# Kernel tuning notes

Measured on AMD Instinct MI355X. Metric: run time of the kernel, lower is better.

## Reference

```python
import jax, jax.numpy as jnp
import numpy as np

B, C, H, W = 4, 96, 256, 256
HEADS = 4
WH = WW = 8            # window size
QKV_D = C // HEADS     # qkv_dim defaults to in_channels // num_heads
N = WH * WW            # tokens per window
EPS = 1e-6


def _rel_index():
    # Swin-style relative position index, [N, N], constant
    coords = np.stack(np.meshgrid(np.arange(WH), np.arange(WW), indexing='ij'), 0).reshape(2, -1)
    rel = coords[:, :, None] - coords[:, None, :]
    rel[0] += WH - 1
    rel[1] += WW - 1
    return rel[0] * (2 * WW - 1) + rel[1]

REL = jnp.asarray(_rel_index())  # int32 [N, N]


def setup_inputs() -> dict:
    key = jax.random.key(0)
    ks = jax.random.split(key, 8)
    s = lambda k, shape: jax.random.normal(k, shape, jnp.float32) * 0.02
    return dict(
        x=jax.random.normal(ks[0], (B, C, H, W), jnp.float32),
        norm_w=jnp.ones((C,), jnp.float32),                      # RMSNorm inside MHA (channel-last tokens)
        qkv_w=s(ks[1], (3 * HEADS * QKV_D, C)),
        qkv_b=jnp.zeros((3 * HEADS * QKV_D,), jnp.float32),
        proj_w=s(ks[2], (C, HEADS * QKV_D)),
        proj_b=jnp.zeros((C,), jnp.float32),
        bias_table=s(ks[3], ((2 * WH - 1) * (2 * WW - 1),)),     # WindowScoreBias table (shared across heads)
        mlp_norm_w=jnp.ones((1, C, 1, 1), jnp.float32),          # RMSNorm1((1,C,1,1), dim=1)
        w1_w=s(ks[4], (2 * C, C, 1, 1)),                         # mid = out_channels*mlp_ratio = 2C
        w1_b=jnp.zeros((2 * C,), jnp.float32),
        w2_w=s(ks[5], (C, C, 3, 3)),                             # mid//2 = C -> C, 3x3
        w2_b=jnp.zeros((C,), jnp.float32),
    )


def rms_norm(x, w, axis):
    v = jnp.mean(x * x, axis=axis, keepdims=True)
    return x * jax.lax.rsqrt(v + EPS) * w


def conv2d(x, w, b):
    y = jax.lax.conv_general_dilated(x, w, (1, 1), 'VALID',
                                     dimension_numbers=('NCHW', 'OIHW', 'NCHW'))
    return y + b[None, :, None, None]


def reference(x, norm_w, qkv_w, qkv_b, proj_w, proj_b, bias_table,
              mlp_norm_w, w1_w, w1_b, w2_w, w2_b):
    B_, C_, H_, W_ = x.shape
    nH, nW = H_ // WH, W_ // WW
    # ---- windowed MHA with norm fused in and relative bias ----
    # window partition: [B,C,H,W] -> [B*nWin, N, C]
    xw = x.reshape(B_, C_, nH, WH, nW, WW).transpose(0, 2, 4, 3, 5, 1).reshape(-1, N, C_)
    xn = rms_norm(xw, norm_w, -1)
    qkv = xn @ qkv_w.T + qkv_b                                  # [Bn, N, 3*h*d]
    qkv = qkv.reshape(-1, N, 3, HEADS, QKV_D).transpose(2, 0, 3, 1, 4)  # [3, Bn, h, N, d]
    q, k, v = qkv[0], qkv[1], qkv[2]
    bias = bias_table[REL]                                      # [N, N], broadcast over batch/heads
    scores = jnp.einsum('bhnd,bhmd->bhnm', q, k) / jnp.sqrt(jnp.float32(QKV_D)) + bias
    attn = jax.nn.softmax(scores, axis=-1)
    o = jnp.einsum('bhnm,bhmd->bhnd', attn, v)
    o = o.transpose(0, 2, 1, 3).reshape(-1, N, HEADS * QKV_D)
    o = o @ proj_w.T + proj_b
    # reverse window partition
    o = o.reshape(B_, nH, nW, WH, WW, C_).transpose(0, 5, 1, 3, 2, 4).reshape(B_, C_, H_, W_)
    x = x + o
    # ---- GLU conv MLP residual ----
    y = rms_norm(x, mlp_norm_w, 1)
    y = conv2d(y, w1_w, w1_b)                                   # 1x1, C -> 2C
    a, g = jnp.split(y, 2, axis=1)
    y = a * jax.nn.sigmoid(g)                                   # GLU along channels
    # ReplicationPad2dDetach: edge pad whose padded ring carries no gradient
    yp = jnp.pad(jax.lax.stop_gradient(y), ((0, 0), (0, 0), (1, 1), (1, 1)), mode='edge')
    yp = yp.at[:, :, 1:-1, 1:-1].set(y)
    y = conv2d(yp, w2_w, w2_b)                                  # 3x3 valid on padded -> same size
    y = jnp.where(y >= 0, y, 0.1 * y)                           # leaky_relu(0.1)
    return x + y
```

## Files before the change

kernel.cpp:

```cpp
#include <hip/hip_runtime.h>
#include <hip/hip_bf16.h>

#define CC 96

typedef short short8  __attribute__((ext_vector_type(8)));
typedef short short4v __attribute__((ext_vector_type(4)));
typedef float f32x4   __attribute__((ext_vector_type(4)));
typedef _Float16 half4 __attribute__((ext_vector_type(4)));

#if __has_builtin(__builtin_amdgcn_mfma_f32_16x16x16_f16)
  #define MFMA16(a,b,c) __builtin_amdgcn_mfma_f32_16x16x16_f16((a),(b),(c),0,0,0)
#else
  #define MFMA16(a,b,c) __builtin_amdgcn_mfma_f32_16x16x16f16((a),(b),(c),0,0,0)
#endif

static __device__ __forceinline__ ushort f2bf(float f) {
  __hip_bfloat16 h = __float2bfloat16(f);
  return *reinterpret_cast<ushort*>(&h);
}
static __device__ __forceinline__ float bf2f(ushort u) {
  union { unsigned int u; float f; } v; v.u = ((unsigned int)u) << 16; return v.f;
}

#define QSCALE 0.20412414523193154f

__global__ void prep_kernel(const float* __restrict__ qkv_w,
                            const float* __restrict__ qkv_b,
                            const float* __restrict__ proj_w,
                            const float* __restrict__ w2w,
                            const float* __restrict__ w1w,
                            __hip_bfloat16* __restrict__ qkvp,
                            float* __restrict__ qkvb2,
                            __hip_bfloat16* __restrict__ projp,
                            __hip_bfloat16* __restrict__ w2p,
                            __hip_bfloat16* __restrict__ w1p,
                            __hip_bfloat16* __restrict__ vwp)
{
  const int i = blockIdx.x*256 + threadIdx.x;
  if (i < 36864) {
    const int e = i & 7, lane = (i >> 3) & 63;
    const int rest = i >> 9;
    const int mt = rest % 6, r2 = rest / 6;
    const int ks = r2 % 3, h = r2 / 3;
    const int od = mt*16 + (lane & 15);
    const int sec = od >> 5, d = od & 31;
    const int c = ks*32 + (lane >> 4)*8 + e;
    float val = 0.f;
    if (d < 24) {
      val = qkv_w[(sec*96 + h*24 + d)*96 + c];
      if (sec == 0) val *= QSCALE;
    }
    qkvp[i] = __float2bfloat16(val);
  }
  const int jb = i - 36864;
  if (jb >= 0 && jb < 384) {
    const int h = jb / 96, od = jb - h*96;
    const int sec = od >> 5, d = od & 31;
    float val = 0.f;
    if (d < 24) {
      val = qkv_b[sec*96 + h*24 + d];
      if (sec == 0) val *= QSCALE;
    }
    qkvb2[jb] = val;
  }
  const int j = i - 37248;
  if (j >= 0 && j < 9216) {
    const int e = j & 7, lane = (j >> 3) & 63;
    const int rest = j >> 9;
    const int nt = rest % 6, ks = rest / 6;
    const int oc = nt*16 + (lane & 15);
    const int dd = ks*32 + (lane >> 4)*8 + e;
    projp[j] = __float2bfloat16(proj_w[oc*96 + dd]);
  }
  const int k = i - 46464;
  if (k >= 0 && k < 82944) {
    const int e = k & 7;
    const int lane = (k >> 3) & 63;
    const int rest = k >> 9;
    const int nf = rest % 6;
    const int r2 = rest / 6;
    const int kc = r2 % 3;
    const int tap = r2 / 3;
    const int cidx = kc*32 + (lane >> 4)*8 + e;
    const int oc = nf*16 + (lane & 15);
    const int ky = tap / 3, kx = tap - ky*3;
    w2p[k] = __float2bfloat16(w2w[((oc*96 + cidx)*3 + ky)*3 + kx]);
  }
  const int m = i - 129408;
  if (m >= 0 && m < 18432) {
    const int e = m & 7, lane = (m >> 3) & 63;
    const int rest = m >> 9;
    const int nt = rest % 12, ks = rest / 12;
    const int oc = nt*16 + (lane & 15);
    const int c  = ks*32 + (lane >> 4)*8 + e;
    w1p[m] = __float2bfloat16(w1w[oc*96 + c]);
  }
  const int v = i - 147840;
  if (v >= 0 && v < 12288) {
    const int e = v & 7, lane = (v >> 3) & 63;
    const int rest = v >> 9;
    const int nt2 = rest % 2, r2 = rest / 2;
    const int ks = r2 % 3, h = r2 / 3;
    const int d = nt2*16 + (lane & 15);
    const int c = ks*32 + (lane >> 4)*8 + e;
    const float val = (d < 24) ? qkv_w[(192 + h*24 + d)*96 + c] : 0.f;
    vwp[v] = __float2bfloat16(val);
  }
}

__global__ __launch_bounds__(512, 2) void attn_kernel(
    const float* __restrict__ x,
    const float* __restrict__ norm_w,
    const __hip_bfloat16* __restrict__ qkvp,
    const float* __restrict__ qkvb2,
    const __hip_bfloat16* __restrict__ vwp,
    const __hip_bfloat16* __restrict__ projp,
    const float* __restrict__ proj_b,
    const float* __restrict__ bias_table,
    float* __restrict__ out)
{
  extern __shared__ char smem[];
  ushort* xn   = (ushort*)smem;
  ushort* xr   = (ushort*)(smem + 26624);
  float*  btab = (float*)(smem + 51200);

  const int wp = blockIdx.x;
  const int b   = wp >> 9;
  const int wy  = (wp >> 4) & 31;
  const int wxp = wp & 15;
  const int t  = threadIdx.x;
  const int y0 = wy*8, x0 = wxp*16;
  const int l  = t & 63;
  const int W  = __builtin_amdgcn_readfirstlane(t >> 6);
  const int w2 = W >> 2, h = W & 3;
  const int lr = l & 15, g = l >> 4;

  for (int i = t; i < 225; i += 512) btab[i] = bias_table[i];

  {
    const int p = t >> 2, q = t & 3;
    const int ty = p >> 4, tx = p & 15;
    const float* xp = x + (size_t)(b*CC + q*24)*65536 + (size_t)(y0+ty)*256 + x0 + tx;
    float xv[24]; float ss = 0.f;
    #pragma unroll
    for (int i = 0; i < 24; i++) { xv[i] = xp[(size_t)i*65536]; ss += xv[i]*xv[i]; }
    ss += __shfl_xor(ss, 1);
    ss += __shfl_xor(ss, 2);
    const float s = rsqrtf(ss * (1.f/96.f) + 1e-6f);
    const int row = (tx >> 3)*64 + ty*8 + (tx & 7);
    #pragma unroll
    for (int k2 = 0; k2 < 3; k2++) {
      short8 pk, pr;
      #pragma unroll
      for (int q2 = 0; q2 < 8; q2++) {
        pr[q2] = (short)f2bf(xv[k2*8+q2]);
        pk[q2] = (short)f2bf(xv[k2*8+q2] * s * norm_w[q*24 + k2*8 + q2]);
      }
      *(short8*)(xn + row*104 + q*24 + k2*8) = pk;
      *(short8*)(xr + row*96  + q*24 + k2*8) = pr;
    }
  }
  __syncthreads();

  half4 qf[2][4], kf[2][4];
  #pragma unroll
  for (int pass = 0; pass < 2; pass++) {
    f32x4 acc[2][4];
    #pragma unroll
    for (int m2 = 0; m2 < 2; m2++)
      #pragma unroll
      for (int nt = 0; nt < 4; nt++) acc[m2][nt] = (f32x4)0.f;
    #pragma unroll
    for (int ks = 0; ks < 3; ks++) {
      short8 bfr[4];
      #pragma unroll
      for (int nt = 0; nt < 4; nt++)
        bfr[nt] = *(const short8*)((const char*)xn + (w2*64 + nt*16 + lr)*208 + g*16 + ks*64);
      #pragma unroll
      for (int m2 = 0; m2 < 2; m2++) {
        const short8 afr = *(const short8*)(qkvp + ((h*3+ks)*6 + pass*2 + m2)*512 + l*8);
        #pragma unroll
        for (int nt = 0; nt < 4; nt++)
          acc[m2][nt] = __builtin_amdgcn_mfma_f32_16x16x32_bf16(afr, bfr[nt], acc[m2][nt], 0, 0, 0);
      }
    }
    #pragma unroll
    for (int m2 = 0; m2 < 2; m2++) {
      const f32x4 bb = *(const f32x4*)(qkvb2 + h*96 + (pass*2+m2)*16 + g*4);
      #pragma unroll
      for (int nt = 0; nt < 4; nt++)
        #pragma unroll
        for (int r = 0; r < 4; r++) {
          const float v = acc[m2][nt][r] + bb[r];
          if (pass == 0) qf[m2][nt][r] = (_Float16)v;
          else           kf[m2][nt][r] = (_Float16)v;
        }
    }
  }

  half4 pa[4][4];
  #pragma unroll
  for (int qt = 0; qt < 4; qt++) {
    f32x4 sacc[4];
    #pragma unroll
    for (int kt = 0; kt < 4; kt++) {
      f32x4 s0 = MFMA16(kf[0][kt], qf[0][qt], (f32x4)0.f);
      sacc[kt] = MFMA16(kf[1][kt], qf[1][qt], s0);
    }
    const int q = qt*16 + lr;
    const int aq = (q >> 3)*15 + (q & 7);
    float vv[4][4];
    float mx = -1e30f;
    #pragma unroll
    for (int kt = 0; kt < 4; kt++)
      #pragma unroll
      for (int r = 0; r < 4; r++) {
        const int k = kt*16 + g*4 + r;
        vv[kt][r] = sacc[kt][r] + btab[aq + 112 - ((k >> 3)*15 + (k & 7))];
        mx = fmaxf(mx, vv[kt][r]);
      }
    mx = fmaxf(mx, __shfl_xor(mx, 16));
    mx = fmaxf(mx, __shfl_xor(mx, 32));
    float sum = 0.f;
    #pragma unroll
    for (int kt = 0; kt < 4; kt++)
      #pragma unroll
      for (int r = 0; r < 4; r++) { vv[kt][r] = __expf(vv[kt][r] - mx); sum += vv[kt][r]; }
    sum += __shfl_xor(sum, 16);
    sum += __shfl_xor(sum, 32);
    const float rinv = 1.f / sum;
    #pragma unroll
    for (int kt = 0; kt < 4; kt++)
      #pragma unroll
      for (int r = 0; r < 4; r++) pa[kt][qt][r] = (_Float16)(vv[kt][r] * rinv);
  }

  half4 vb[4][2];
  {
    f32x4 vacc[4][2];
    #pragma unroll
    for (int kt = 0; kt < 4; kt++) { vacc[kt][0] = (f32x4)0.f; vacc[kt][1] = (f32x4)0.f; }
    #pragma unroll
    for (int ks = 0; ks < 3; ks++) {
      short8 afr[4];
      #pragma unroll
      for (int kt = 0; kt < 4; kt++)
        afr[kt] = *(const short8*)((const char*)xn + (w2*64 + kt*16 + lr)*208 + g*16 + ks*64);
      #pragma unroll
      for (int nt2 = 0; nt2 < 2; nt2++) {
        const short8 vwf = *(const short8*)(vwp + ((h*3+ks)*2+nt2)*512 + l*8);
        #pragma unroll
        for (int kt = 0; kt < 4; kt++)
          vacc[kt][nt2] = __builtin_amdgcn_mfma_f32_16x16x32_bf16(afr[kt], vwf, vacc[kt][nt2], 0, 0, 0);
      }
    }
    #pragma unroll
    for (int nt2 = 0; nt2 < 2; nt2++) {
      const float vbias = qkvb2[h*96 + 64 + nt2*16 + lr];
      #pragma unroll
      for (int kt = 0; kt < 4; kt++)
        #pragma unroll
        for (int r = 0; r < 4; r++)
          vb[kt][nt2][r] = (_Float16)(vacc[kt][nt2][r] + vbias);
    }
  }

  f32x4 oacc[4][2];
  #pragma unroll
  for (int qt = 0; qt < 4; qt++) { oacc[qt][0] = (f32x4)0.f; oacc[qt][1] = (f32x4)0.f; }
  #pragma unroll
  for (int kt = 0; kt < 4; kt++)
    #pragma unroll
    for (int qt = 0; qt < 4; qt++) {
      oacc[qt][0] = MFMA16(pa[kt][qt], vb[kt][0], oacc[qt][0]);
      oacc[qt][1] = MFMA16(pa[kt][qt], vb[kt][1], oacc[qt][1]);
    }
  __syncthreads();

  #pragma unroll
  for (int qt = 0; qt < 4; qt++)
    #pragma unroll
    for (int r = 0; r < 4; r++) {
      const int row = w2*64 + qt*16 + g*4 + r;
      xn[row*104 + h*24 + lr] = f2bf(oacc[qt][0][r]);
      if (lr < 8) xn[row*104 + h*24 + 16 + lr] = f2bf(oacc[qt][1][r]);
    }
  __syncthreads();

  {
    f32x4 pacc[6];
    #pragma unroll
    for (int nt = 0; nt < 6; nt++) pacc[nt] = (f32x4)0.f;
    #pragma unroll
    for (int ks = 0; ks < 3; ks++) {
      const short8 af = *(const short8*)((const char*)xn + (lr + W*16)*208 + g*16 + ks*64);
      #pragma unroll
      for (int nt = 0; nt < 6; nt++) {
        const short8 bf = *(const short8*)(projp + (ks*6+nt)*512 + l*8);
        pacc[nt] = __builtin_amdgcn_mfma_f32_16x16x32_bf16(af, bf, pacc[nt], 0, 0, 0);
      }
    }
    __syncthreads();
    ushort* oT = xn;
    #pragma unroll
    for (int nt = 0; nt < 6; nt++) {
      const int oc = lr + nt*16;
      const float bias = proj_b[oc];
      short4v pk;
      #pragma unroll
      for (int r = 0; r < 4; r++) {
        const int row = W*16 + g*4 + r;
        pk[r] = (short)f2bf(pacc[nt][r] + bias + bf2f(xr[row*96 + oc]));
      }
      *(short4v*)((char*)oT + oc*264 + (g*4 + W*16)*2) = pk;
    }
  }
  __syncthreads();

  {
    const ushort* oT = xn;
    #pragma unroll
    for (int k2 = 0; k2 < 6; k2++) {
      const int e = t + k2*512;
      const int oc = e >> 5, q5 = e & 31;
      const int ty = q5 >> 2, tq = q5 & 3;
      const int m = (tq >> 1)*64 + ty*8 + (tq & 1)*4;
      const short4v ov = *(const short4v*)((const char*)oT + oc*264 + m*2);
      const size_t gidx = (size_t)(b*CC+oc)*65536 + (size_t)(y0+ty)*256 + x0 + tq*4;
      float4 res;
      res.x = bf2f((ushort)ov[0]);
      res.y = bf2f((ushort)ov[1]);
      res.z = bf2f((ushort)ov[2]);
      res.w = bf2f((ushort)ov[3]);
      *(float4*)(out + gidx) = res;
    }
  }
}

__global__ __launch_bounds__(256, 2) void mlp1_kernel(
    const float* __restrict__ x1,
    const float* __restrict__ mlp_norm_w,
    const __hip_bfloat16* __restrict__ w1p,
    const float* __restrict__ w1_b,
    __hip_bfloat16* __restrict__ y)
{
  __shared__ ushort xn[128*104];
  const int blk = blockIdx.x;
  const int b   = blk >> 9;
  const int p0  = (blk & 511) << 7;
  const int t   = threadIdx.x;
  const int l   = t & 63;
  const int w   = __builtin_amdgcn_readfirstlane(t >> 6);
  const int lr  = l & 15, g = l >> 4;

  {
    const int p = t >> 1, half = t & 1;
    const float* xp = x1 + (size_t)(b*CC + half*48)*65536 + p0 + p;
    float xv[48];
    float ss = 0.f;
    #pragma unroll
    for (int i = 0; i < 48; i++) { xv[i] = xp[(size_t)i*65536]; ss += xv[i]*xv[i]; }
    ss += __shfl_xor(ss, 1);
    const float s = rsqrtf(ss*(1.f/96.f) + 1e-6f);
    #pragma unroll
    for (int i = 0; i < 48; i += 2) {
      const int c = half*48 + i;
      union { ushort u[2]; uint v; } pk;
      pk.u[0] = f2bf(xv[i]   * s * mlp_norm_w[c]);
      pk.u[1] = f2bf(xv[i+1] * s * mlp_norm_w[c+1]);
      *(uint*)(&xn[p*104 + c]) = pk.v;
    }
  }

  f32x4 acc[2][12];
  #pragma unroll
  for (int m2 = 0; m2 < 2; m2++)
    #pragma unroll
    for (int nt = 0; nt < 12; nt++) acc[m2][nt] = (f32x4)0.f;

  #pragma unroll
  for (int ks = 0; ks < 3; ks++) {
    short8 afr[2];
    #pragma unroll
    for (int m2 = 0; m2 < 2; m2++)
      afr[m2] = *(const short8*)((const char*)xn + (lr + (w*2+m2)*16)*208 + g*16 + ks*64);
    #pragma unroll
    for (int nt = 0; nt < 12; nt++) {
      const short8 bfr = *(const short8*)(w1p + ((ks*12+nt)*64 + l)*8);
      #pragma unroll
      for (int m2 = 0; m2 < 2; m2++)
        acc[m2][nt] = __builtin_amdgcn_mfma_f32_16x16x32_bf16(afr[m2], bfr, acc[m2][nt], 0, 0, 0);
    }
  }

  #pragma unroll
  for (int m2 = 0; m2 < 2; m2++)
    #pragma unroll
    for (int nt = 0; nt < 6; nt++) {
      const int oc = nt*16 + lr;
      const float ab = w1_b[oc], gb = w1_b[96+oc];
      #pragma unroll
      for (int r = 0; r < 4; r++) {
        const int row = (w*2+m2)*16 + g*4 + r;
        const float a  = acc[m2][nt][r]   + ab;
        const float gg = acc[m2][nt+6][r] + gb;
        xn[row*104 + oc] = f2bf(a / (1.f + __expf(-gg)));
      }
    }
  __syncthreads();

  __hip_bfloat16* yp = y + ((size_t)(b*65536 + p0))*96;
  #pragma unroll
  for (int k2 = 0; k2 < 6; k2++) {
    const int e = t + k2*256;
    const int p = e / 12, ch = e - p*12;
    const short8 v = *(const short8*)(&xn[p*104 + ch*8]);
    *(short8*)((ushort*)yp + p*96 + ch*8) = v;
  }
}

__global__ __launch_bounds__(256) void conv3_kernel(
    const __hip_bfloat16* __restrict__ y,
    const __hip_bfloat16* __restrict__ w2p,
    const float* __restrict__ w2_b,
    float* __restrict__ xout)
{
  extern __shared__ char smem[];
  ushort* A = (ushort*)smem;
  float*  O = (float*)smem;

  const int bid = blockIdx.x;
  const int b   = bid >> 9;
  const int rp  = (bid >> 2) & 127;
  const int ch  = bid & 3;
  const int px0 = ch << 6;
  const int t   = threadIdx.x;
  const int w   = __builtin_amdgcn_readfirstlane(t >> 6);
  const int l   = t & 63;
  const int m15 = l & 15, lh = l >> 4;

  for (int e = t; e < 3168; e += 256) {
    const int seg  = e / 12;
    const int part = e - seg*12;
    const int ky = seg / 66;
    const int px = seg - ky*66;
    const int gy = min(255, max(0, 2*rp + ky - 1));
    const int gx = min(255, max(0, px0 + px - 1));
    const short8 v = *(const short8*)(y + ((size_t)(b*65536 + gy*256 + gx))*96 + part*8);
    *(short8*)(A + seg*104 + part*8) = v;
  }
  __syncthreads();

  f32x4 acc0[6], acc1[6];
  #pragma unroll
  for (int nf = 0; nf < 6; ++nf) { acc0[nf] = (f32x4)0.f; acc1[nf] = (f32x4)0.f; }

  for (int tap = 0; tap < 9; ++tap) {
    const int ky = tap / 3, kx = tap - ky*3;
    for (int kc = 0; kc < 3; ++kc) {
      const int cb = kc*32 + lh*8;
      const short8 a0 = *(const short8*)(A + ((ky  )*66 + 16*w + m15 + kx)*104 + cb);
      const short8 a1 = *(const short8*)(A + ((ky+1)*66 + 16*w + m15 + kx)*104 + cb);
      const short8* bp = (const short8*)w2p + ((size_t)(tap*3 + kc)*6)*64 + l;
      #pragma unroll
      for (int nf = 0; nf < 6; ++nf) {
        const short8 bf = bp[nf*64];
        acc0[nf] = __builtin_amdgcn_mfma_f32_16x16x32_bf16(a0, bf, acc0[nf], 0, 0, 0);
        acc1[nf] = __builtin_amdgcn_mfma_f32_16x16x32_bf16(a1, bf, acc1[nf], 0, 0, 0);
      }
    }
  }
  __syncthreads();

  {
    const int jb = 16*w + lh*4;
    #pragma unroll
    for (int nf = 0; nf < 6; ++nf) {
      const int oc = nf*16 + m15;
      *(f32x4*)(O + oc*132 + jb)      = acc0[nf];
      *(f32x4*)(O + oc*132 + 64 + jb) = acc1[nf];
    }
  }
  __syncthreads();

  for (int e = t; e < 3072; e += 256) {
    const int oc = e >> 5;
    const int j  = (e & 31) * 4;
    f32x4 v = *(const f32x4*)(O + oc*132 + j);
    const float bb = w2_b[oc];
    const int gy = 2*rp + (j >> 6);
    const int px = px0 + (j & 63);
    float* op = xout + ((size_t)(b*CC + oc))*65536 + (size_t)gy*256 + px;
    f32x4 r = *(const f32x4*)op;
    #pragma unroll
    for (int q = 0; q < 4; ++q) {
      float u = v[q] + bb;
      u = (u >= 0.f) ? u : 0.1f*u;
      r[q] += u;
    }
    *(f32x4*)op = r;
  }
}

extern "C" void kernel_launch(void* const* d_in, const int* in_sizes, int n_in,
                              void* d_out, int out_size, void* d_ws, size_t ws_size,
                              hipStream_t stream)
{
  (void)in_sizes; (void)n_in; (void)out_size; (void)ws_size;
  const float* x      = (const float*)d_in[0];
  const float* norm_w = (const float*)d_in[1];
  const float* qkv_w  = (const float*)d_in[2];
  const float* qkv_b  = (const float*)d_in[3];
  const float* proj_w = (const float*)d_in[4];
  const float* proj_b = (const float*)d_in[5];
  const float* btab   = (const float*)d_in[6];
  const float* mlpnw  = (const float*)d_in[7];
  const float* w1w    = (const float*)d_in[8];
  const float* w1b    = (const float*)d_in[9];
  const float* w2w    = (const float*)d_in[10];
  const float* w2b    = (const float*)d_in[11];
  float* out = (float*)d_out;

  char* ws = (char*)d_ws;
  __hip_bfloat16* y     = (__hip_bfloat16*)ws;
  __hip_bfloat16* w2p   = (__hip_bfloat16*)(ws + 50331648);
  __hip_bfloat16* qkvp  = (__hip_bfloat16*)(ws + 50497536);
  float*          qkvb2 = (float*)(ws + 50571264);
  __hip_bfloat16* projp = (__hip_bfloat16*)(ws + 50572800);
  __hip_bfloat16* w1p   = (__hip_bfloat16*)(ws + 50591232);
  __hip_bfloat16* vwp   = (__hip_bfloat16*)(ws + 50628096);

  prep_kernel<<<626, 256, 0, stream>>>(qkv_w, qkv_b, proj_w, w2w, w1w,
                                       qkvp, qkvb2, projp, w2p, w1p, vwp);

  attn_kernel<<<2048, 512, 52100, stream>>>(x, norm_w, qkvp, qkvb2, vwp, projp, proj_b, btab, out);
  mlp1_kernel<<<2048, 256, 0, stream>>>(out, mlpnw, w1p, w1b, y);
  conv3_kernel<<<2048, 256, 54912, stream>>>(y, w2p, w2b, out);
}
```

Measured before the change: 269.8 us.

## Restructure conv3 to 8 waves per block with direct-from-register epilogue

The 3x3 conv kernel now runs 512 threads per block, with each wave computing a single 16-pixel row segment instead of two rows. The LDS staging round-trip for the output transpose is removed, so results go straight from MFMA accumulators to global memory. Residual values are prefetched into registers before the main loop. Block IDs are also remapped so that consecutive blocks spread across batch and column chunks. The aim is more waves in flight, fewer barriers and lower register pressure, at the cost of each wave reusing its B-fragment loads over only one A row.

```diff
diff --git a/kernel.cpp b/kernel.cpp
--- a/kernel.cpp
+++ b/kernel.cpp
@@ -419,7 +419,7 @@
   }
 }
 
-__global__ __launch_bounds__(256) void conv3_kernel(
+__global__ __launch_bounds__(512, 4) void conv3_kernel(
     const __hip_bfloat16* __restrict__ y,
     const __hip_bfloat16* __restrict__ w2p,
     const float* __restrict__ w2_b,
@@ -427,19 +427,21 @@
 {
   extern __shared__ char smem[];
   ushort* A = (ushort*)smem;
-  float*  O = (float*)smem;
-
-  const int bid = blockIdx.x;
-  const int b   = bid >> 9;
-  const int rp  = (bid >> 2) & 127;
-  const int ch  = bid & 3;
+
+  const int vbid = (blockIdx.x & 7)*256 + (blockIdx.x >> 3);
+  const int b   = vbid >> 9;
+  const int rem = vbid & 511;
+  const int ch  = rem >> 7;
+  const int rp  = rem & 127;
   const int px0 = ch << 6;
   const int t   = threadIdx.x;
-  const int w   = __builtin_amdgcn_readfirstlane(t >> 6);
+  const int W   = __builtin_amdgcn_readfirstlane(t >> 6);
+  const int rw  = W & 1;
+  const int pw  = W >> 1;
   const int l   = t & 63;
   const int m15 = l & 15, lh = l >> 4;
 
-  for (int e = t; e < 3168; e += 256) {
+  for (int e = t; e < 3168; e += 512) {
     const int seg  = e / 12;
     const int part = e - seg*12;
     const int ky = seg / 66;
@@ -449,52 +451,42 @@
     const short8 v = *(const short8*)(y + ((size_t)(b*65536 + gy*256 + gx))*96 + part*8);
     *(short8*)(A + seg*104 + part*8) = v;
   }
+
+  const int gyo  = 2*rp + rw;
+  const int gpx  = px0 + 16*pw + lh*4;
+  f32x4 resid[6];
+  #pragma unroll
+  for (int nf = 0; nf < 6; nf++) {
+    const int oc = nf*16 + m15;
+    resid[nf] = *(const f32x4*)(xout + ((size_t)(b*CC + oc))*65536 + (size_t)gyo*256 + gpx);
+  }
   __syncthreads();
 
-  f32x4 acc0[6], acc1[6];
-  #pragma unroll
-  for (int nf = 0; nf < 6; ++nf) { acc0[nf] = (f32x4)0.f; acc1[nf] = (f32x4)0.f; }
+  f32x4 acc[6];
+  #pragma unroll
+  for (int nf = 0; nf < 6; ++nf) acc[nf] = (f32x4)0.f;
 
   for (int tap = 0; tap < 9; ++tap) {
     const int ky = tap / 3, kx = tap - ky*3;
     for (int kc = 0; kc < 3; ++kc) {
       const int cb = kc*32 + lh*8;
-      const short8 a0 = *(const short8*)(A + ((ky  )*66 + 16*w + m15 + kx)*104 + cb);
-      const short8 a1 = *(const short8*)(A + ((ky+1)*66 + 16*w + m15 + kx)*104 + cb);
+      const short8 a0 = *(const short8*)(A + ((ky + rw)*66 + 16*pw + m15 + kx)*104 + cb);
       const short8* bp = (const short8*)w2p + ((size_t)(tap*3 + kc)*6)*64 + l;
       #pragma unroll
-      for (int nf = 0; nf < 6; ++nf) {
-        const short8 bf = bp[nf*64];
-        acc0[nf] = __builtin_amdgcn_mfma_f32_16x16x32_bf16(a0, bf, acc0[nf], 0, 0, 0);
-        acc1[nf] = __builtin_amdgcn_mfma_f32_16x16x32_bf16(a1, bf, acc1[nf], 0, 0, 0);
-      }
-    }
-  }
-  __syncthreads();
-
-  {
-    const int jb = 16*w + lh*4;
-    #pragma unroll
-    for (int nf = 0; nf < 6; ++nf) {
-      const int oc = nf*16 + m15;
-      *(f32x4*)(O + oc*132 + jb)      = acc0[nf];
-      *(f32x4*)(O + oc*132 + 64 + jb) = acc1[nf];
-    }
-  }
-  __syncthreads();
-
-  for (int e = t; e < 3072; e += 256) {
-    const int oc = e >> 5;
-    const int j  = (e & 31) * 4;
-    f32x4 v = *(const f32x4*)(O + oc*132 + j);
+      for (int nf = 0; nf < 6; ++nf)
+        acc[nf] = __builtin_amdgcn_mfma_f32_16x16x32_bf16(a0, bp[nf*64], acc[nf], 0, 0, 0);
+    }
+  }
+
+  #pragma unroll
+  for (int nf = 0; nf < 6; ++nf) {
+    const int oc = nf*16 + m15;
     const float bb = w2_b[oc];
-    const int gy = 2*rp + (j >> 6);
-    const int px = px0 + (j & 63);
-    float* op = xout + ((size_t)(b*CC + oc))*65536 + (size_t)gy*256 + px;
-    f32x4 r = *(const f32x4*)op;
+    float* op = xout + ((size_t)(b*CC + oc))*65536 + (size_t)gyo*256 + gpx;
+    f32x4 r = resid[nf];
     #pragma unroll
     for (int q = 0; q < 4; ++q) {
-      float u = v[q] + bb;
+      float u = acc[nf][q] + bb;
       u = (u >= 0.f) ? u : 0.1f*u;
       r[q] += u;
     }
@@ -535,5 +527,5 @@
 
   attn_kernel<<<2048, 512, 52100, stream>>>(x, norm_w, qkvp, qkvb2, vwp, projp, proj_b, btab, out);
   mlp1_kernel<<<2048, 256, 0, stream>>>(out, mlpnw, w1p, w1b, y);
-  conv3_kernel<<<2048, 256, 54912, stream>>>(y, w2p, w2b, out);
-}
+  conv3_kernel<<<2048, 512, 54912, stream>>>(y, w2p, w2b, out);
+}
```

Result: no change. 266.2 us (-1.3%).
